# Kernel tuning notes

Hardware: AMD Instinct MI355X
Metric: run time of the kernel (lower is better)

The kernel has to match this reference:

```python
import jax, jax.numpy as jnp
import numpy as np

B = 4
N0, N1, N2 = 32768, 8192, 2048
C0, C1, C2 = 256, 512, 1024
EPS = 1e-5  # torch BatchNorm1d default eps


def _mlp(x, w1, b1, g, be, w2, b2):
    # Linear -> BatchNorm1d (training-mode batch stats over B and N) -> ReLU -> Linear
    h = x @ w1 + b1                      # (B, N, H)
    mu = jnp.mean(h, axis=(0, 1))
    var = jnp.mean((h - mu) ** 2, axis=(0, 1))  # biased var, as torch BN uses for normalization
    h = jax.nn.relu((h - mu) * jax.lax.rsqrt(var + EPS) * g + be)
    return h @ w2 + b2


def _gather(feats, idx):
    # feats: (B, N_coarse, C), idx: (B, N_fine) -> (B, N_fine, C)
    return jax.vmap(lambda f, i: f[i])(feats, idx)


def _lin(key, fan_in, fan_out, scale=0.02):
    return jax.random.normal(key, (fan_in, fan_out), dtype=jnp.float32) * scale


def setup_inputs() -> dict:
    key = jax.random.key(0)
    ks = jax.random.split(key, 16)
    inp = {
        'f0': jax.random.normal(ks[0], (B, N0, C0), dtype=jnp.float32),
        'f1': jax.random.normal(ks[1], (B, N1, C1), dtype=jnp.float32),
        'f2': jax.random.normal(ks[2], (B, N2, C2), dtype=jnp.float32),
        # up_mlps[0]: MLP(C1, [C1, C0])
        'up0_w1': _lin(ks[3], C1, C1), 'up0_b1': jnp.zeros((C1,), jnp.float32),
        'up0_g': jnp.ones((C1,), jnp.float32), 'up0_be': jnp.zeros((C1,), jnp.float32),
        'up0_w2': _lin(ks[4], C1, C0), 'up0_b2': jnp.zeros((C0,), jnp.float32),
        # up_mlps[1]: MLP(C2, [C2, C1])
        'up1_w1': _lin(ks[5], C2, C2), 'up1_b1': jnp.zeros((C2,), jnp.float32),
        'up1_g': jnp.ones((C2,), jnp.float32), 'up1_be': jnp.zeros((C2,), jnp.float32),
        'up1_w2': _lin(ks[6], C2, C1), 'up1_b2': jnp.zeros((C1,), jnp.float32),
        # skip_mlps[0]: MLP(2*C0, [2*C0, C0])
        'skip0_w1': _lin(ks[7], 2 * C0, 2 * C0), 'skip0_b1': jnp.zeros((2 * C0,), jnp.float32),
        'skip0_g': jnp.ones((2 * C0,), jnp.float32), 'skip0_be': jnp.zeros((2 * C0,), jnp.float32),
        'skip0_w2': _lin(ks[8], 2 * C0, C0), 'skip0_b2': jnp.zeros((C0,), jnp.float32),
        # skip_mlps[1]: MLP(2*C1, [2*C1, C1])
        'skip1_w1': _lin(ks[9], 2 * C1, 2 * C1), 'skip1_b1': jnp.zeros((2 * C1,), jnp.float32),
        'skip1_g': jnp.ones((2 * C1,), jnp.float32), 'skip1_be': jnp.zeros((2 * C1,), jnp.float32),
        'skip1_w2': _lin(ks[10], 2 * C1, C1), 'skip1_b2': jnp.zeros((C1,), jnp.float32),
        'pool0': jax.random.randint(ks[11], (B, N0), 0, N1, dtype=jnp.int32),
        'pool1': jax.random.randint(ks[12], (B, N1), 0, N2, dtype=jnp.int32),
    }
    return inp


def reference(f0, f1, f2,
              up0_w1, up0_b1, up0_g, up0_be, up0_w2, up0_b2,
              up1_w1, up1_b1, up1_g, up1_be, up1_w2, up1_b2,
              skip0_w1, skip0_b1, skip0_g, skip0_be, skip0_w2, skip0_b2,
              skip1_w1, skip1_b1, skip1_g, skip1_be, skip1_w2, skip1_b2,
              pool0, pool1):
    # start at coarsest level
    x = f2                                               # (B, N2, C2)
    # level i = 1
    x = _mlp(x, up1_w1, up1_b1, up1_g, up1_be, up1_w2, up1_b2)   # (B, N2, C1)
    x = _gather(x, pool1)                                 # (B, N1, C1)
    x = _mlp(jnp.concatenate([f1, x], axis=-1),
             skip1_w1, skip1_b1, skip1_g, skip1_be, skip1_w2, skip1_b2)  # (B, N1, C1)
    # level i = 0
    x = _mlp(x, up0_w1, up0_b1, up0_g, up0_be, up0_w2, up0_b2)   # (B, N1, C0)
    x = _gather(x, pool0)                                 # (B, N0, C0)
    x = _mlp(jnp.concatenate([f0, x], axis=-1),
             skip0_w1, skip0_b1, skip0_g, skip0_be, skip0_w2, skip0_b2)  # (B, N0, C0)
    return x
```

## Files before the change

### kernel.cpp

```cpp
#include <hip/hip_runtime.h>


typedef unsigned short u16;
typedef __attribute__((ext_vector_type(8))) short bf16x8;
typedef __attribute__((ext_vector_type(4))) float f32x4;

#define EPW 136

__device__ __forceinline__ float b2f(u16 u) {
    union { unsigned int i; float f; } v; v.i = ((unsigned int)u) << 16; return v.f;
}
__device__ __forceinline__ u16 f2b(float f) {
    union { float f; unsigned int i; } v; v.f = f;
    unsigned int r = v.i + 0x7FFFu + ((v.i >> 16) & 1u);
    return (u16)(r >> 16);
}

__device__ __forceinline__ void gld_lds16(const u16* g, u16* l) {
    __builtin_amdgcn_global_load_lds(
        (const __attribute__((address_space(1))) unsigned int*)g,
        (__attribute__((address_space(3))) unsigned int*)l,
        16, 0, 0);
}

union SMem {
    struct { u16 a[128 * 64]; u16 b[128 * 64]; } st;
    u16 ep[128 * EPW];
};

template <bool AFFINE_A, bool STATS, bool OUT_F32, bool GATHER>
__global__ __launch_bounds__(256) void gemm_bn(
    const u16* __restrict__ A, const u16* __restrict__ BT, void* __restrict__ Cout,
    const float* __restrict__ scale, const float* __restrict__ shift,
    const float* __restrict__ bias,
    float* __restrict__ psum, float* __restrict__ psumsq,
    const u16* __restrict__ Xg, const int* __restrict__ pool,
    int nfShift, int Nc, int Chalf,
    int N, int K)
{
    __shared__ __align__(16) SMem sm;

    const int tid  = threadIdx.x;
    const int w    = tid >> 6;
    const int lane = tid & 63;
    const int wm   = w & 1, wn = w >> 1;

    int bm, bn;
    {
        const int flat = (int)(blockIdx.y * gridDim.x + blockIdx.x);
        const int xcd  = flat & 7;
        const int s    = flat >> 3;
        const int nbn  = (int)gridDim.x;
        const int lb   = 31 - __builtin_clz(nbn);
        bn = s & (nbn - 1);
        bm = xcd * ((int)gridDim.y >> 3) + (s >> lb);
    }

    const int scol = (lane & 7) * 8;
    const u16* Bg = BT + (size_t)(bn * 128 + w * 32 + (lane >> 3)) * K + scol;

    const u16* agA[4];
    const u16* agX[4];
    if constexpr (GATHER) {
#pragma unroll
        for (int q = 0; q < 4; q++) {
            const int row = bm * 128 + w * 32 + q * 8 + (lane >> 3);
            const int b   = row >> nfShift;
            const int p   = pool[row];
            agA[q] = A  + (size_t)row * Chalf + scol;
            agX[q] = Xg + ((size_t)b * Nc + p) * Chalf + scol;
        }
    } else {
#pragma unroll
        for (int q = 0; q < 4; q++)
            agA[q] = A + (size_t)(bm * 128 + w * 32 + q * 8 + (lane >> 3)) * K + scol;
    }

    f32x4 acc[4][4];
    const f32x4 zero = {0.f, 0.f, 0.f, 0.f};
#pragma unroll
    for (int i = 0; i < 4; i++)
#pragma unroll
        for (int j = 0; j < 4; j++) acc[i][j] = zero;

    const int nkt = K >> 6;
    for (int kt = 0; kt < nkt; kt++) {
        const int kof = kt * 64;
#pragma unroll
        for (int q = 0; q < 4; q++)
            gld_lds16(Bg + (size_t)(q * 8) * K + kof, &sm.st.b[(w * 32 + q * 8) * 64]);
        if constexpr (GATHER) {
            if (kof < Chalf) {
#pragma unroll
                for (int q = 0; q < 4; q++)
                    gld_lds16(agA[q] + kof, &sm.st.a[(w * 32 + q * 8) * 64]);
            } else {
#pragma unroll
                for (int q = 0; q < 4; q++)
                    gld_lds16(agX[q] + (kof - Chalf), &sm.st.a[(w * 32 + q * 8) * 64]);
            }
        } else if constexpr (!AFFINE_A) {
#pragma unroll
            for (int q = 0; q < 4; q++)
                gld_lds16(agA[q] + kof, &sm.st.a[(w * 32 + q * 8) * 64]);
        } else {
            const float4 sc0 = *(const float4*)(scale + kof + scol);
            const float4 sc1 = *(const float4*)(scale + kof + scol + 4);
            const float4 sh0 = *(const float4*)(shift + kof + scol);
            const float4 sh1 = *(const float4*)(shift + kof + scol + 4);
#pragma unroll
            for (int q = 0; q < 4; q++) {
                union { uint4 u; u16 s[8]; } r, o;
                r.u = *(const uint4*)(agA[q] + kof);
                o.s[0] = f2b(fmaxf(b2f(r.s[0]) * sc0.x + sh0.x, 0.f));
                o.s[1] = f2b(fmaxf(b2f(r.s[1]) * sc0.y + sh0.y, 0.f));
                o.s[2] = f2b(fmaxf(b2f(r.s[2]) * sc0.z + sh0.z, 0.f));
                o.s[3] = f2b(fmaxf(b2f(r.s[3]) * sc0.w + sh0.w, 0.f));
                o.s[4] = f2b(fmaxf(b2f(r.s[4]) * sc1.x + sh1.x, 0.f));
                o.s[5] = f2b(fmaxf(b2f(r.s[5]) * sc1.y + sh1.y, 0.f));
                o.s[6] = f2b(fmaxf(b2f(r.s[6]) * sc1.z + sh1.z, 0.f));
                o.s[7] = f2b(fmaxf(b2f(r.s[7]) * sc1.w + sh1.w, 0.f));
                *(uint4*)&sm.st.a[(w * 32 + q * 8 + (lane >> 3)) * 64 + scol] = o.u;
            }
        }
        __syncthreads();
#pragma unroll
        for (int ks = 0; ks < 2; ks++) {
            const int kk = ks * 32 + (lane >> 4) * 8;
            bf16x8 af[4], bfr[4];
#pragma unroll
            for (int i = 0; i < 4; i++)
                af[i] = *(const bf16x8*)&sm.st.a[(wm * 64 + i * 16 + (lane & 15)) * 64 + kk];
#pragma unroll
            for (int j = 0; j < 4; j++)
                bfr[j] = *(const bf16x8*)&sm.st.b[(wn * 64 + j * 16 + (lane & 15)) * 64 + kk];
#pragma unroll
            for (int i = 0; i < 4; i++)
#pragma unroll
                for (int j = 0; j < 4; j++)
                    acc[i][j] = __builtin_amdgcn_mfma_f32_16x16x32_bf16(af[i], bfr[j], acc[i][j], 0, 0, 0);
        }
        __syncthreads();
    }

    const int cl = lane & 15, quad = lane >> 4;
#pragma unroll
    for (int j = 0; j < 4; j++) {
        const int colLocal = wn * 64 + j * 16 + cl;
        const int col = bn * 128 + colLocal;
        float bcol = 0.f;
        if constexpr (!STATS) bcol = bias[col];
        float s = 0.f, ss = 0.f;
#pragma unroll
        for (int i = 0; i < 4; i++) {
            const int rowLocal0 = wm * 64 + i * 16 + quad * 4;
#pragma unroll
            for (int r = 0; r < 4; r++) {
                const float v = acc[i][j][r];
                if constexpr (STATS) { s += v; ss += v * v; }
                const float o = v + bcol;
                if constexpr (OUT_F32)
                    ((float*)Cout)[(size_t)(bm * 128 + rowLocal0 + r) * N + col] = o;
                else
                    sm.ep[(rowLocal0 + r) * EPW + colLocal] = f2b(o);
            }
        }
        if constexpr (STATS) {
            s  += __shfl_xor(s, 16);  s  += __shfl_xor(s, 32);
            ss += __shfl_xor(ss, 16); ss += __shfl_xor(ss, 32);
            if (quad == 0) { atomicAdd(&psum[col], s); atomicAdd(&psumsq[col], ss); }
        }
    }
    if constexpr (!OUT_F32) {
        __syncthreads();
        u16* Cb = (u16*)Cout;
#pragma unroll
        for (int it = 0; it < 8; it++) {
            const int row = it * 16 + (tid >> 4);
            const int c8  = (tid & 15) * 8;
            const uint4 v = *(const uint4*)&sm.ep[row * EPW + c8];
            *(uint4*)(Cb + (size_t)(bm * 128 + row) * N + bn * 128 + c8) = v;
        }
    }
}

__global__ void cvt_transpose_w(const float* __restrict__ W, u16* __restrict__ WT, int K, int N) {
    __shared__ float t[32][33];
    const int tx = threadIdx.x, ty = threadIdx.y;
    const int n0 = blockIdx.x * 32, k0 = blockIdx.y * 32;
#pragma unroll
    for (int r = 0; r < 4; r++)
        t[ty + r * 8][tx] = W[(size_t)(k0 + ty + r * 8) * N + n0 + tx];
    __syncthreads();
#pragma unroll
    for (int r = 0; r < 4; r++)
        WT[(size_t)(n0 + ty + r * 8) * K + k0 + tx] = f2b(t[tx][ty + r * 8]);
}

__global__ void cvt_f32_bf16(const float* __restrict__ x, u16* __restrict__ y, long n8) {
    const long t = (long)blockIdx.x * 256 + threadIdx.x;
    if (t >= n8) return;
    const float4 a = ((const float4*)x)[t * 2];
    const float4 b = ((const float4*)x)[t * 2 + 1];
    union { uint4 u; u16 s[8]; } o;
    o.s[0] = f2b(a.x); o.s[1] = f2b(a.y); o.s[2] = f2b(a.z); o.s[3] = f2b(a.w);
    o.s[4] = f2b(b.x); o.s[5] = f2b(b.y); o.s[6] = f2b(b.z); o.s[7] = f2b(b.w);
    ((uint4*)y)[t] = o.u;
}

__global__ void bn_finalize(const float* __restrict__ sum, const float* __restrict__ sumsq,
                            const float* __restrict__ g, const float* __restrict__ be,
                            float* __restrict__ scale, float* __restrict__ shift,
                            int Cc, float invM) {
    const int c = blockIdx.x * 256 + threadIdx.x;
    if (c >= Cc) return;
    const float mu = sum[c] * invM;
    const float var = fmaf(sumsq[c], invM, -mu * mu);
    const float sc = g[c] * rsqrtf(var + 1e-5f);
    scale[c] = sc;
    shift[c] = fmaf(-mu, sc, be[c]);
}

extern "C" void kernel_launch(void* const* d_in, const int* in_sizes, int n_in,
                              void* d_out, int out_size, void* d_ws, size_t ws_size,
                              hipStream_t stream) {
    const float* f0     = (const float*)d_in[0];
    const float* f1     = (const float*)d_in[1];
    const float* f2     = (const float*)d_in[2];
    const float* up0_w1 = (const float*)d_in[3];
    const float* up0_g  = (const float*)d_in[5];
    const float* up0_be = (const float*)d_in[6];
    const float* up0_w2 = (const float*)d_in[7];
    const float* up0_b2 = (const float*)d_in[8];
    const float* up1_w1 = (const float*)d_in[9];
    const float* up1_g  = (const float*)d_in[11];
    const float* up1_be = (const float*)d_in[12];
    const float* up1_w2 = (const float*)d_in[13];
    const float* up1_b2 = (const float*)d_in[14];
    const float* sk0_w1 = (const float*)d_in[15];
    const float* sk0_g  = (const float*)d_in[17];
    const float* sk0_be = (const float*)d_in[18];
    const float* sk0_w2 = (const float*)d_in[19];
    const float* sk0_b2 = (const float*)d_in[20];
    const float* sk1_w1 = (const float*)d_in[21];
    const float* sk1_g  = (const float*)d_in[23];
    const float* sk1_be = (const float*)d_in[24];
    const float* sk1_w2 = (const float*)d_in[25];
    const float* sk1_b2 = (const float*)d_in[26];
    const int* pool0    = (const int*)d_in[27];
    const int* pool1    = (const int*)d_in[28];
    float* out = (float*)d_out;

    char* ws = (char*)d_ws;
    size_t off = 0;
    auto alloc = [&](size_t bytes) -> void* {
        void* p = ws + off;
        off += (bytes + 255) & ~(size_t)255;
        return p;
    };
    u16* w_up1_1 = (u16*)alloc((size_t)1024 * 1024 * 2);
    u16* w_up1_2 = (u16*)alloc((size_t)512 * 1024 * 2);
    u16* w_sk1_1 = (u16*)alloc((size_t)1024 * 1024 * 2);
    u16* w_sk1_2 = (u16*)alloc((size_t)512 * 1024 * 2);
    u16* w_up0_1 = (u16*)alloc((size_t)512 * 512 * 2);
    u16* w_up0_2 = (u16*)alloc((size_t)256 * 512 * 2);
    u16* w_sk0_1 = (u16*)alloc((size_t)512 * 512 * 2);
    u16* w_sk0_2 = (u16*)alloc((size_t)256 * 512 * 2);
    float* stats = (float*)alloc((size_t)4 * 4096 * 4);
    u16* Hbuf    = (u16*)alloc((size_t)131072 * 512 * 2);
    u16* Xbuf    = (u16*)alloc((size_t)32768 * 512 * 2);
    u16* f0b     = (u16*)alloc((size_t)4 * 32768 * 256 * 2);
    u16* f1b     = (u16*)alloc((size_t)4 * 8192 * 512 * 2);
    u16* f2b_    = (u16*)alloc((size_t)4 * 2048 * 1024 * 2);

    const dim3 tb(32, 8);
    cvt_transpose_w<<<dim3(32, 32), tb, 0, stream>>>(up1_w1, w_up1_1, 1024, 1024);
    cvt_transpose_w<<<dim3(16, 32), tb, 0, stream>>>(up1_w2, w_up1_2, 1024, 512);
    cvt_transpose_w<<<dim3(32, 32), tb, 0, stream>>>(sk1_w1, w_sk1_1, 1024, 1024);
    cvt_transpose_w<<<dim3(16, 32), tb, 0, stream>>>(sk1_w2, w_sk1_2, 1024, 512);
    cvt_transpose_w<<<dim3(16, 16), tb, 0, stream>>>(up0_w1, w_up0_1, 512, 512);
    cvt_transpose_w<<<dim3(8, 16),  tb, 0, stream>>>(up0_w2, w_up0_2, 512, 256);
    cvt_transpose_w<<<dim3(16, 16), tb, 0, stream>>>(sk0_w1, w_sk0_1, 512, 512);
    cvt_transpose_w<<<dim3(8, 16),  tb, 0, stream>>>(sk0_w2, w_sk0_2, 512, 256);

    hipMemsetAsync(stats, 0, (size_t)4 * 4096 * sizeof(float), stream);
    cvt_f32_bf16<<<4096,  256, 0, stream>>>(f2, f2b_, 8388608L / 8);
    cvt_f32_bf16<<<8192,  256, 0, stream>>>(f1, f1b, 16777216L / 8);
    cvt_f32_bf16<<<16384, 256, 0, stream>>>(f0, f0b, 33554432L / 8);

    float* st0 = stats;
    float* st1 = stats + 4096;
    float* st2 = stats + 8192;
    float* st3 = stats + 12288;

    gemm_bn<false, true, false, false><<<dim3(8, 64), 256, 0, stream>>>(
        f2b_, w_up1_1, Hbuf, nullptr, nullptr, nullptr, st0, st0 + 1024,
        nullptr, nullptr, 0, 0, 0, 1024, 1024);
    bn_finalize<<<4, 256, 0, stream>>>(st0, st0 + 1024, up1_g, up1_be, st0 + 2048, st0 + 3072, 1024, 1.f / 8192.f);
    gemm_bn<true, false, false, false><<<dim3(4, 64), 256, 0, stream>>>(
        Hbuf, w_up1_2, Xbuf, st0 + 2048, st0 + 3072, up1_b2, nullptr, nullptr,
        nullptr, nullptr, 0, 0, 0, 512, 1024);

    gemm_bn<false, true, false, true><<<dim3(8, 256), 256, 0, stream>>>(
        f1b, w_sk1_1, Hbuf, nullptr, nullptr, nullptr, st1, st1 + 1024,
        Xbuf, pool1, 13, 2048, 512, 1024, 1024);
    bn_finalize<<<4, 256, 0, stream>>>(st1, st1 + 1024, sk1_g, sk1_be, st1 + 2048, st1 + 3072, 1024, 1.f / 32768.f);
    gemm_bn<true, false, false, false><<<dim3(4, 256), 256, 0, stream>>>(
        Hbuf, w_sk1_2, Xbuf, st1 + 2048, st1 + 3072, sk1_b2, nullptr, nullptr,
        nullptr, nullptr, 0, 0, 0, 512, 1024);

    gemm_bn<false, true, false, false><<<dim3(4, 256), 256, 0, stream>>>(
        Xbuf, w_up0_1, Hbuf, nullptr, nullptr, nullptr, st2, st2 + 1024,
        nullptr, nullptr, 0, 0, 0, 512, 512);
    bn_finalize<<<2, 256, 0, stream>>>(st2, st2 + 1024, up0_g, up0_be, st2 + 2048, st2 + 3072, 512, 1.f / 32768.f);
    gemm_bn<true, false, false, false><<<dim3(2, 256), 256, 0, stream>>>(
        Hbuf, w_up0_2, Xbuf, st2 + 2048, st2 + 3072, up0_b2, nullptr, nullptr,
        nullptr, nullptr, 0, 0, 0, 256, 512);

    gemm_bn<false, true, false, true><<<dim3(4, 1024), 256, 0, stream>>>(
        f0b, w_sk0_1, Hbuf, nullptr, nullptr, nullptr, st3, st3 + 1024,
        Xbuf, pool0, 15, 8192, 256, 512, 512);
    bn_finalize<<<2, 256, 0, stream>>>(st3, st3 + 1024, sk0_g, sk0_be, st3 + 2048, st3 + 3072, 512, 1.f / 131072.f);
    gemm_bn<true, false, true, false><<<dim3(2, 1024), 256, 0, stream>>>(
        Hbuf, w_sk0_2, out, st3 + 2048, st3 + 3072, sk0_b2, nullptr, nullptr,
        nullptr, nullptr, 0, 0, 0, 256, 512);
}
```

Measured before the change: 881.6 us.

## Rewrite GEMM as 256x256 double-buffered ping-pong pipeline with swizzled LDS

```diff
diff --git a/kernel.cpp b/kernel.cpp
--- a/kernel.cpp
+++ b/kernel.cpp
@@ -5,7 +5,8 @@
 typedef __attribute__((ext_vector_type(8))) short bf16x8;
 typedef __attribute__((ext_vector_type(4))) float f32x4;
 
-#define EPW 136
+#define UNROLL _Pragma("unroll")
+#define EPW 264
 
 __device__ __forceinline__ float b2f(u16 u) {
     union { unsigned int i; float f; } v; v.i = ((unsigned int)u) << 16; return v.f;
@@ -23,13 +24,19 @@
         16, 0, 0);
 }
 
+#define VMCNT(n) asm volatile("s_waitcnt vmcnt(" #n ")" ::: "memory")
+#define LGKM0    asm volatile("s_waitcnt lgkmcnt(0)" ::: "memory")
+#define BAR()    do{ asm volatile("" ::: "memory"); \
+                     __builtin_amdgcn_s_barrier(); \
+                     asm volatile("" ::: "memory"); }while(0)
+
 union SMem {
-    struct { u16 a[128 * 64]; u16 b[128 * 64]; } st;
-    u16 ep[128 * EPW];
+    struct { u16 a[2][256 * 64]; u16 b[2][256 * 64]; float ss[2048]; } st;
+    u16 ep[256 * EPW];
 };
 
 template <bool AFFINE_A, bool STATS, bool OUT_F32, bool GATHER>
-__global__ __launch_bounds__(256) void gemm_bn(
+__global__ __launch_bounds__(512, 2) void gemm_bn(
     const u16* __restrict__ A, const u16* __restrict__ BT, void* __restrict__ Cout,
     const float* __restrict__ scale, const float* __restrict__ shift,
     const float* __restrict__ bias,
@@ -43,145 +50,227 @@
     const int tid  = threadIdx.x;
     const int w    = tid >> 6;
     const int lane = tid & 63;
-    const int wm   = w & 1, wn = w >> 1;
+    const int wm   = w >> 2, wn = w & 3;
+    const int l15  = lane & 15;
+    const int xorv = (lane & 7) << 3;
+    const int swz8 = ((lane & 7) ^ (lane >> 3)) << 3;
+    const int kS0  = (((lane >> 4) << 3)) ^ xorv;
+    const int kS1  = (32 + ((lane >> 4) << 3)) ^ xorv;
 
     int bm, bn;
     {
+        const int nbn  = (int)gridDim.x;
+        const int nwg  = nbn * (int)gridDim.y;
         const int flat = (int)(blockIdx.y * gridDim.x + blockIdx.x);
-        const int xcd  = flat & 7;
-        const int s    = flat >> 3;
-        const int nbn  = (int)gridDim.x;
+        const int wg   = (flat & 7) * (nwg >> 3) + (flat >> 3);
         const int lb   = 31 - __builtin_clz(nbn);
-        bn = s & (nbn - 1);
-        bm = xcd * ((int)gridDim.y >> 3) + (s >> lb);
-    }
-
-    const int scol = (lane & 7) * 8;
-    const u16* Bg = BT + (size_t)(bn * 128 + w * 32 + (lane >> 3)) * K + scol;
-
-    const u16* agA[4];
-    const u16* agX[4];
-    if constexpr (GATHER) {
-#pragma unroll
-        for (int q = 0; q < 4; q++) {
-            const int row = bm * 128 + w * 32 + q * 8 + (lane >> 3);
-            const int b   = row >> nfShift;
-            const int p   = pool[row];
-            agA[q] = A  + (size_t)row * Chalf + scol;
-            agX[q] = Xg + ((size_t)b * Nc + p) * Chalf + scol;
+        bn = wg & (nbn - 1);
+        bm = wg >> lb;
+    }
+
+    const u16* aS[2][2]; const u16* xS[2][2]; const u16* bS[2][2];
+    int dA[2][2], dB[2][2], wIdx[2][2];
+    UNROLL for (int u = 0; u < 2; u++)
+    UNROLL for (int ld = 0; ld < 2; ld++) {
+        const int urb = w * 16 + ld * 8;
+        const int ur  = urb + (lane >> 3);
+        {
+            const int trb = urb + (urb >= 64 ? 64 : 0) + u * 64;
+            const int tr  = ur  + (ur  >= 64 ? 64 : 0) + u * 64;
+            dA[u][ld] = trb * 64;
+            const int rowG = bm * 256 + tr;
+            if constexpr (GATHER) {
+                const int b = rowG >> nfShift;
+                const int p = pool[rowG];
+                aS[u][ld] = A  + (size_t)rowG * Chalf + swz8;
+                xS[u][ld] = Xg + ((size_t)b * Nc + p) * Chalf + swz8;
+            } else if constexpr (AFFINE_A) {
+                aS[u][ld] = A + (size_t)rowG * K + ((lane & 7) << 3);
+                wIdx[u][ld] = tr * 64 + swz8;
+            } else {
+                aS[u][ld] = A + (size_t)rowG * K + swz8;
+            }
+        }
+        {
+            const int trb = ((urb >> 5) << 6) + (urb & 31) + u * 32;
+            const int tr  = ((ur  >> 5) << 6) + (ur  & 31) + u * 32;
+            dB[u][ld] = trb * 64;
+            bS[u][ld] = BT + (size_t)(bn * 256 + tr) * K + swz8;
+        }
+    }
+
+    f32x4 acc[8][4];
+    const f32x4 zero = {0.f, 0.f, 0.f, 0.f};
+    UNROLL for (int i = 0; i < 8; i++)
+    UNROLL for (int j = 0; j < 4; j++) acc[i][j] = zero;
+    bf16x8 afr[4][2];
+    bf16x8 bfr[2][2][2];
+    uint4 rA[2][2];
+
+#define STAGE_A_(u, nb, KOF) do{ \
+    if constexpr (AFFINE_A) { \
+        rA[u][0] = *(const uint4*)(aS[u][0] + (KOF)); \
+        rA[u][1] = *(const uint4*)(aS[u][1] + (KOF)); \
+    } else if constexpr (GATHER) { \
+        const u16 *s0_, *s1_; \
+        if ((KOF) < Chalf) { s0_ = aS[u][0] + (KOF); s1_ = aS[u][1] + (KOF); } \
+        else { s0_ = xS[u][0] + ((KOF) - Chalf); s1_ = xS[u][1] + ((KOF) - Chalf); } \
+        gld_lds16(s0_, &sm.st.a[(nb)][dA[u][0]]); \
+        gld_lds16(s1_, &sm.st.a[(nb)][dA[u][1]]); \
+    } else { \
+        gld_lds16(aS[u][0] + (KOF), &sm.st.a[(nb)][dA[u][0]]); \
+        gld_lds16(aS[u][1] + (KOF), &sm.st.a[(nb)][dA[u][1]]); \
+    } }while(0)
+
+#define STAGE_B_(u, nb, KOF) do{ \
+    gld_lds16(bS[u][0] + (KOF), &sm.st.b[(nb)][dB[u][0]]); \
+    gld_lds16(bS[u][1] + (KOF), &sm.st.b[(nb)][dB[u][1]]); }while(0)
+
+#define AFF_WRITE_(u, tb, KOF) do{ if constexpr (AFFINE_A) { \
+    const int kb_ = (KOF) + ((lane & 7) << 3); \
+    const float4 sc0_ = *(const float4*)&sm.st.ss[kb_]; \
+    const float4 sc1_ = *(const float4*)&sm.st.ss[kb_ + 4]; \
+    const float4 sh0_ = *(const float4*)&sm.st.ss[1024 + kb_]; \
+    const float4 sh1_ = *(const float4*)&sm.st.ss[1024 + kb_ + 4]; \
+    UNROLL for (int ld_ = 0; ld_ < 2; ld_++) { \
+        union { uint4 u4; u16 s[8]; } r_, o_; r_.u4 = rA[u][ld_]; \
+        o_.s[0] = f2b(fmaxf(b2f(r_.s[0]) * sc0_.x + sh0_.x, 0.f)); \
+        o_.s[1] = f2b(fmaxf(b2f(r_.s[1]) * sc0_.y + sh0_.y, 0.f)); \
+        o_.s[2] = f2b(fmaxf(b2f(r_.s[2]) * sc0_.z + sh0_.z, 0.f)); \
+        o_.s[3] = f2b(fmaxf(b2f(r_.s[3]) * sc0_.w + sh0_.w, 0.f)); \
+        o_.s[4] = f2b(fmaxf(b2f(r_.s[4]) * sc1_.x + sh1_.x, 0.f)); \
+        o_.s[5] = f2b(fmaxf(b2f(r_.s[5]) * sc1_.y + sh1_.y, 0.f)); \
+        o_.s[6] = f2b(fmaxf(b2f(r_.s[6]) * sc1_.z + sh1_.z, 0.f)); \
+        o_.s[7] = f2b(fmaxf(b2f(r_.s[7]) * sc1_.w + sh1_.w, 0.f)); \
+        *(uint4*)&sm.st.a[(tb)][wIdx[u][ld_]] = o_.u4; } \
+    LGKM0; } }while(0)
+
+#define READ_A(buf, qi) do{ const u16* p_ = sm.st.a[(buf)]; \
+    UNROLL for (int i_ = 0; i_ < 4; i_++) { \
+        const int rb_ = (wm * 128 + ((qi) * 4 + i_) * 16 + l15) * 64; \
+        afr[i_][0] = *(const bf16x8*)&p_[rb_ + kS0]; \
+        afr[i_][1] = *(const bf16x8*)&p_[rb_ + kS1]; } }while(0)
+
+#define READ_B(buf, qj) do{ const u16* p_ = sm.st.b[(buf)]; \
+    UNROLL for (int j_ = 0; j_ < 2; j_++) { \
+        const int rb_ = (wn * 64 + ((qj) * 2 + j_) * 16 + l15) * 64; \
+        bfr[qj][j_][0] = *(const bf16x8*)&p_[rb_ + kS0]; \
+        bfr[qj][j_][1] = *(const bf16x8*)&p_[rb_ + kS1]; } }while(0)
+
+#define MFMA_Q(qi, qj) do{ __builtin_amdgcn_s_setprio(1); \
+    UNROLL for (int i_ = 0; i_ < 4; i_++) \
+    UNROLL for (int j_ = 0; j_ < 2; j_++) { \
+        acc[(qi)*4+i_][(qj)*2+j_] = __builtin_amdgcn_mfma_f32_16x16x32_bf16( \
+            afr[i_][0], bfr[qj][j_][0], acc[(qi)*4+i_][(qj)*2+j_], 0, 0, 0); \
+        acc[(qi)*4+i_][(qj)*2+j_] = __builtin_amdgcn_mfma_f32_16x16x32_bf16( \
+            afr[i_][1], bfr[qj][j_][1], acc[(qi)*4+i_][(qj)*2+j_], 0, 0, 0); } \
+    __builtin_amdgcn_s_setprio(0); }while(0)
+
+    const int nkt = K >> 6;
+
+    if constexpr (AFFINE_A) {
+        for (int i = tid; i < K; i += 512) {
+            sm.st.ss[i] = scale[i]; sm.st.ss[1024 + i] = shift[i];
+        }
+    }
+    STAGE_A_(0, 0, 0); STAGE_B_(0, 0, 0); STAGE_B_(1, 0, 0); STAGE_A_(1, 0, 0);
+    asm volatile("s_waitcnt vmcnt(0) lgkmcnt(0)" ::: "memory");
+    BAR();
+    if constexpr (AFFINE_A) { AFF_WRITE_(0, 0, 0); BAR(); }
+
+    for (int t = 0; t < nkt - 1; ++t) {
+        const int buf = t & 1, nb = buf ^ 1;
+        const int kofN = (t + 1) << 6;
+        STAGE_A_(0, nb, kofN);
+        READ_A(buf, 0);
+        READ_B(buf, 0);
+        BAR();
+        MFMA_Q(0, 0);
+        STAGE_B_(0, nb, kofN);
+        VMCNT(6);
+        BAR();
+        READ_B(buf, 1);
+        MFMA_Q(0, 1);
+        STAGE_B_(1, nb, kofN);
+        VMCNT(6);
+        AFF_WRITE_(1, buf, t << 6);
+        BAR();
+        READ_A(buf, 1);
+        MFMA_Q(1, 1);
+        STAGE_A_(1, nb, kofN);
+        BAR();
+        MFMA_Q(1, 0);
+        VMCNT(4);
+        AFF_WRITE_(0, nb, kofN);
+        BAR();
+    }
+
+    {
+        const int t = nkt - 1, buf = t & 1;
+        READ_A(buf, 0);
+        READ_B(buf, 0);
+        BAR();
+        MFMA_Q(0, 0);
+        VMCNT(2);
+        BAR();
+        READ_B(buf, 1);
+        MFMA_Q(0, 1);
+        VMCNT(0);
+        AFF_WRITE_(1, buf, t << 6);
+        BAR();
+        READ_A(buf, 1);
+        MFMA_Q(1, 1);
+        BAR();
+        MFMA_Q(1, 0);
+    }
+
+    const int cl = l15, quad = lane >> 4;
+    if constexpr (OUT_F32) {
+        UNROLL for (int j = 0; j < 4; j++) {
+            const int col = bn * 256 + wn * 64 + j * 16 + cl;
+            const float bcol = bias[col];
+            UNROLL for (int i = 0; i < 8; i++) {
+                const int r0 = bm * 256 + wm * 128 + i * 16 + quad * 4;
+                UNROLL for (int r = 0; r < 4; r++)
+                    ((float*)Cout)[(size_t)(r0 + r) * N + col] = acc[i][j][r] + bcol;
+            }
         }
     } else {
-#pragma unroll
-        for (int q = 0; q < 4; q++)
-            agA[q] = A + (size_t)(bm * 128 + w * 32 + q * 8 + (lane >> 3)) * K + scol;
-    }
-
-    f32x4 acc[4][4];
-    const f32x4 zero = {0.f, 0.f, 0.f, 0.f};
-#pragma unroll
-    for (int i = 0; i < 4; i++)
-#pragma unroll
-        for (int j = 0; j < 4; j++) acc[i][j] = zero;
-
-    const int nkt = K >> 6;
-    for (int kt = 0; kt < nkt; kt++) {
-        const int kof = kt * 64;
-#pragma unroll
-        for (int q = 0; q < 4; q++)
-            gld_lds16(Bg + (size_t)(q * 8) * K + kof, &sm.st.b[(w * 32 + q * 8) * 64]);
-        if constexpr (GATHER) {
-            if (kof < Chalf) {
-#pragma unroll
-                for (int q = 0; q < 4; q++)
-                    gld_lds16(agA[q] + kof, &sm.st.a[(w * 32 + q * 8) * 64]);
-            } else {
-#pragma unroll
-                for (int q = 0; q < 4; q++)
-                    gld_lds16(agX[q] + (kof - Chalf), &sm.st.a[(w * 32 + q * 8) * 64]);
+        UNROLL for (int j = 0; j < 4; j++) {
+            const int colL = wn * 64 + j * 16 + cl;
+            const int col = bn * 256 + colL;
+            float bcol = 0.f;
+            if constexpr (!STATS) bcol = bias[col];
+            float s = 0.f, ss2 = 0.f;
+            UNROLL for (int i = 0; i < 8; i++) {
+                const int rL0 = wm * 128 + i * 16 + quad * 4;
+                UNROLL for (int r = 0; r < 4; r++) {
+                    const float v = acc[i][j][r];
+                    if constexpr (STATS) { s += v; ss2 += v * v; }
+                    sm.ep[(rL0 + r) * EPW + colL] = f2b(v + bcol);
+                }
             }
-        } else if constexpr (!AFFINE_A) {
-#pragma unroll
-            for (int q = 0; q < 4; q++)
-                gld_lds16(agA[q] + kof, &sm.st.a[(w * 32 + q * 8) * 64]);
-        } else {
-            const float4 sc0 = *(const float4*)(scale + kof + scol);
-            const float4 sc1 = *(const float4*)(scale + kof + scol + 4);
-            const float4 sh0 = *(const float4*)(shift + kof + scol);
-            const float4 sh1 = *(const float4*)(shift + kof + scol + 4);
-#pragma unroll
-            for (int q = 0; q < 4; q++) {
-                union { uint4 u; u16 s[8]; } r, o;
-                r.u = *(const uint4*)(agA[q] + kof);
-                o.s[0] = f2b(fmaxf(b2f(r.s[0]) * sc0.x + sh0.x, 0.f));
-                o.s[1] = f2b(fmaxf(b2f(r.s[1]) * sc0.y + sh0.y, 0.f));
-                o.s[2] = f2b(fmaxf(b2f(r.s[2]) * sc0.z + sh0.z, 0.f));
-                o.s[3] = f2b(fmaxf(b2f(r.s[3]) * sc0.w + sh0.w, 0.f));
-                o.s[4] = f2b(fmaxf(b2f(r.s[4]) * sc1.x + sh1.x, 0.f));
-                o.s[5] = f2b(fmaxf(b2f(r.s[5]) * sc1.y + sh1.y, 0.f));
-                o.s[6] = f2b(fmaxf(b2f(r.s[6]) * sc1.z + sh1.z, 0.f));
-                o.s[7] = f2b(fmaxf(b2f(r.s[7]) * sc1.w + sh1.w, 0.f));
-                *(uint4*)&sm.st.a[(w * 32 + q * 8 + (lane >> 3)) * 64 + scol] = o.u;
+            if constexpr (STATS) {
+                s   += __shfl_xor(s, 16);   s   += __shfl_xor(s, 32);
+                ss2 += __shfl_xor(ss2, 16); ss2 += __shfl_xor(ss2, 32);
+                if (quad == 0) { atomicAdd(&psum[col], s); atomicAdd(&psumsq[col], ss2); }
             }
         }
-        __syncthreads();
-#pragma unroll
-        for (int ks = 0; ks < 2; ks++) {
-            const int kk = ks * 32 + (lane >> 4) * 8;
-            bf16x8 af[4], bfr[4];
-#pragma unroll
-            for (int i = 0; i < 4; i++)
-                af[i] = *(const bf16x8*)&sm.st.a[(wm * 64 + i * 16 + (lane & 15)) * 64 + kk];
-#pragma unroll
-            for (int j = 0; j < 4; j++)
-                bfr[j] = *(const bf16x8*)&sm.st.b[(wn * 64 + j * 16 + (lane & 15)) * 64 + kk];
-#pragma unroll
-            for (int i = 0; i < 4; i++)
-#pragma unroll
-                for (int j = 0; j < 4; j++)
-                    acc[i][j] = __builtin_amdgcn_mfma_f32_16x16x32_bf16(af[i], bfr[j], acc[i][j], 0, 0, 0);
-        }
-        __syncthreads();
-    }
-
-    const int cl = lane & 15, quad = lane >> 4;
-#pragma unroll
-    for (int j = 0; j < 4; j++) {
-        const int colLocal = wn * 64 + j * 16 + cl;
-        const int col = bn * 128 + colLocal;
-        float bcol = 0.f;
-        if constexpr (!STATS) bcol = bias[col];
-        float s = 0.f, ss = 0.f;
-#pragma unroll
-        for (int i = 0; i < 4; i++) {
-            const int rowLocal0 = wm * 64 + i * 16 + quad * 4;
-#pragma unroll
-            for (int r = 0; r < 4; r++) {
-                const float v = acc[i][j][r];
-                if constexpr (STATS) { s += v; ss += v * v; }
-                const float o = v + bcol;
-                if constexpr (OUT_F32)
-                    ((float*)Cout)[(size_t)(bm * 128 + rowLocal0 + r) * N + col] = o;
-                else
-                    sm.ep[(rowLocal0 + r) * EPW + colLocal] = f2b(o);
-            }
-        }
-        if constexpr (STATS) {
-            s  += __shfl_xor(s, 16);  s  += __shfl_xor(s, 32);
-            ss += __shfl_xor(ss, 16); ss += __shfl_xor(ss, 32);
-            if (quad == 0) { atomicAdd(&psum[col], s); atomicAdd(&psumsq[col], ss); }
-        }
-    }
-    if constexpr (!OUT_F32) {
         __syncthreads();
         u16* Cb = (u16*)Cout;
-#pragma unroll
-        for (int it = 0; it < 8; it++) {
-            const int row = it * 16 + (tid >> 4);
-            const int c8  = (tid & 15) * 8;
+        UNROLL for (int it = 0; it < 16; it++) {
+            const int row = it * 16 + (tid >> 5);
+            const int c8  = (tid & 31) * 8;
             const uint4 v = *(const uint4*)&sm.ep[row * EPW + c8];
-            *(uint4*)(Cb + (size_t)(bm * 128 + row) * N + bn * 128 + c8) = v;
-        }
-    }
+            *(uint4*)(Cb + (size_t)(bm * 256 + row) * N + bn * 256 + c8) = v;
+        }
+    }
+#undef STAGE_A_
+#undef STAGE_B_
+#undef AFF_WRITE_
+#undef READ_A
+#undef READ_B
+#undef MFMA_Q
 }
 
 __global__ void cvt_transpose_w(const float* __restrict__ W, u16* __restrict__ WT, int K, int N) {
@@ -293,35 +382,35 @@
     float* st2 = stats + 8192;
     float* st3 = stats + 12288;
 
-    gemm_bn<false, true, false, false><<<dim3(8, 64), 256, 0, stream>>>(
+    gemm_bn<false, true, false, false><<<dim3(4, 32), 512, 0, stream>>>(
         f2b_, w_up1_1, Hbuf, nullptr, nullptr, nullptr, st0, st0 + 1024,
         nullptr, nullptr, 0, 0, 0, 1024, 1024);
     bn_finalize<<<4, 256, 0, stream>>>(st0, st0 + 1024, up1_g, up1_be, st0 + 2048, st0 + 3072, 1024, 1.f / 8192.f);
-    gemm_bn<true, false, false, false><<<dim3(4, 64), 256, 0, stream>>>(
+    gemm_bn<true, false, false, false><<<dim3(2, 32), 512, 0, stream>>>(
         Hbuf, w_up1_2, Xbuf, st0 + 2048, st0 + 3072, up1_b2, nullptr, nullptr,
         nullptr, nullptr, 0, 0, 0, 512, 1024);
 
-    gemm_bn<false, true, false, true><<<dim3(8, 256), 256, 0, stream>>>(
+    gemm_bn<false, true, false, true><<<dim3(4, 128), 512, 0, stream>>>(
         f1b, w_sk1_1, Hbuf, nullptr, nullptr, nullptr, st1, st1 + 1024,
         Xbuf, pool1, 13, 2048, 512, 1024, 1024);
     bn_finalize<<<4, 256, 0, stream>>>(st1, st1 + 1024, sk1_g, sk1_be, st1 + 2048, st1 + 3072, 1024, 1.f / 32768.f);
-    gemm_bn<true, false, false, false><<<dim3(4, 256), 256, 0, stream>>>(
+    gemm_bn<true, false, false, false><<<dim3(2, 128), 512, 0, stream>>>(
         Hbuf, w_sk1_2, Xbuf, st1 + 2048, st1 + 3072, sk1_b2, nullptr, nullptr,
         nullptr, nullptr, 0, 0, 0, 512, 1024);
 
-    gemm_bn<false, true, false, false><<<dim3(4, 256), 256, 0, stream>>>(
+    gemm_bn<false, true, false, false><<<dim3(2, 128), 512, 0, stream>>>(
         Xbuf, w_up0_1, Hbuf, nullptr, nullptr, nullptr, st2, st2 + 1024,
         nullptr, nullptr, 0, 0, 0, 512, 512);
     bn_finalize<<<2, 256, 0, stream>>>(st2, st2 + 1024, up0_g, up0_be, st2 + 2048, st2 + 3072, 512, 1.f / 32768.f);
-    gemm_bn<true, false, false, false><<<dim3(2, 256), 256, 0, stream>>>(
+    gemm_bn<true, false, false, false><<<dim3(1, 128), 512, 0, stream>>>(
         Hbuf, w_up0_2, Xbuf, st2 + 2048, st2 + 3072, up0_b2, nullptr, nullptr,
         nullptr, nullptr, 0, 0, 0, 256, 512);
 
-    gemm_bn<false, true, false, true><<<dim3(4, 1024), 256, 0, stream>>>(
+    gemm_bn<false, true, false, true><<<dim3(2, 512), 512, 0, stream>>>(
         f0b, w_sk0_1, Hbuf, nullptr, nullptr, nullptr, st3, st3 + 1024,
         Xbuf, pool0, 15, 8192, 256, 512, 512);
     bn_finalize<<<2, 256, 0, stream>>>(st3, st3 + 1024, sk0_g, sk0_be, st3 + 2048, st3 + 3072, 512, 1.f / 131072.f);
-    gemm_bn<true, false, true, false><<<dim3(2, 1024), 256, 0, stream>>>(
+    gemm_bn<true, false, true, false><<<dim3(1, 512), 512, 0, stream>>>(
         Hbuf, w_sk0_2, out, st3 + 2048, st3 + 3072, sk0_b2, nullptr, nullptr,
         nullptr, nullptr, 0, 0, 0, 256, 512);
 }
```

Result: faster. 831.1 us (-5.7%).
